# Performance work log

Measured on AMD Instinct MI355X. Metric: run time of the kernel, lower is better.

Reference implementation:

```python
import jax, jax.numpy as jnp
import numpy as np

N, E, D, H_ATT = 10000, 640000, 128, 64


def setup_inputs() -> dict:
    key = jax.random.key(0)
    ks = jax.random.split(key, 8)
    s = 1.0 / np.sqrt(D)
    return {
        "x": jax.random.normal(ks[0], (N, D), jnp.float32),
        "row": jax.random.randint(ks[1], (E,), 0, N, dtype=jnp.int32),
        "col": jax.random.randint(ks[2], (E,), 0, N, dtype=jnp.int32),
        "W1": jax.random.normal(ks[3], (D, D), jnp.float32) * s,
        "b1": jnp.zeros((D,), jnp.float32),
        "W2": jax.random.normal(ks[4], (D, D), jnp.float32) * s,
        "b2": jnp.zeros((D,), jnp.float32),
        "A1": jax.random.normal(ks[5], (D, H_ATT), jnp.float32) * s,
        "ab1": jnp.zeros((H_ATT,), jnp.float32),
        "A2": jax.random.normal(ks[6], (H_ATT, 1), jnp.float32) * (1.0 / np.sqrt(H_ATT)),
    }


def _cos_sim(a, b):
    # torch.cosine_similarity with eps=1e-8
    num = jnp.sum(a * b, axis=-1)
    den = jnp.maximum(jnp.linalg.norm(a, axis=-1) * jnp.linalg.norm(b, axis=-1), 1e-8)
    return num / den


def _euclid(a, b):
    # nn.PairwiseDistance(p=2)
    return jnp.sqrt(jnp.sum((a - b) ** 2, axis=-1) + 1e-12)


def _gcn(x, ew, row, col, W, b):
    # PyG GCNConv: add self loops (weight 1), symmetric normalization, SpMM.
    n = x.shape[0]
    loop = jnp.arange(n, dtype=row.dtype)
    r = jnp.concatenate([row, loop])  # target
    c = jnp.concatenate([col, loop])  # source
    w = jnp.concatenate([ew, jnp.ones((n,), x.dtype)])
    deg = jax.ops.segment_sum(w, r, num_segments=n)
    dis = jnp.where(deg > 0, jax.lax.rsqrt(jnp.maximum(deg, 1e-12)), 0.0)
    norm = dis[r] * w * dis[c]  # [E+N]
    h = x @ W  # [N, out]
    out = jax.ops.segment_sum(norm[:, None] * h[c], r, num_segments=n)
    return out + b


def reference(x, row, col, W1, b1, W2, b2, A1, ab1, A2):
    # --- cosine branch ---
    w = _cos_sim(x[row], x[col])
    x1 = jax.nn.relu(_gcn(x, w, row, col, W1, b1))
    w = _cos_sim(x1[row], x1[col])
    x1 = _gcn(x1, w, row, col, W2, b2)
    # --- euclidean branch ---
    w = _euclid(x[row], x[col])
    x2 = jax.nn.relu(_gcn(x, w, row, col, W1, b1))
    w = _euclid(x2[row], x2[col])
    x2 = _gcn(x2, w, row, col, W2, b2)
    # --- semantic attention fusion ---
    emb = jnp.stack([x1, x2], axis=1)  # [N, 2, D]
    score = jnp.tanh(emb @ A1 + ab1) @ A2  # [N, 2, 1]
    beta = jax.nn.softmax(score, axis=1)
    return jnp.sum(beta * emb, axis=1)  # [N, D]
```

## Files before the change

### kernel.cpp

```cpp
#include <hip/hip_runtime.h>
#include <cstdint>
#include <cstddef>

#define DF 128
#define HATT 64
#define SL 64
#define RPB 1280

static inline int divup(int a, int b) { return (a + b - 1) / b; }

typedef int vint4 __attribute__((ext_vector_type(4)));

__device__ __forceinline__ void warm_table(const float* t, int nf4, int b, int nb) {
    int slice = (nf4 + nb - 1) / nb;
    int start = b * slice;
    int end = min(start + slice, nf4);
    float acc = 0.f;
    for (int i = start + (int)threadIdx.x; i < end; i += 256) {
        float4 v = ((const float4*)t)[i];
        acc += v.x + v.y + v.z + v.w;
    }
    asm volatile("" :: "v"(acc));
}

__device__ __forceinline__ void hist2_body(int bid, const int* __restrict__ row,
                                           int* __restrict__ cnt2,
                                           int E, int n, int ranges, int rpb, int es) {
    int rb = bid % ranges;
    int s  = bid / ranges;
    int lo = rb * rpb, hi = min(lo + rpb, n);
    int rows = hi - lo;
    __shared__ int lc[RPB];
    for (int j = threadIdx.x; j < rows; j += 256) lc[j] = 0;
    __syncthreads();
    int i0 = s * es, i1 = min(i0 + es, E);
    const vint4* rv = (const vint4*)row;
    for (int j = i0 / 4 + threadIdx.x; j < i1 / 4; j += 256) {
        vint4 r4 = __builtin_nontemporal_load(rv + j);
        if (r4.x >= lo && r4.x < hi) atomicAdd(&lc[r4.x - lo], 1);
        if (r4.y >= lo && r4.y < hi) atomicAdd(&lc[r4.y - lo], 1);
        if (r4.z >= lo && r4.z < hi) atomicAdd(&lc[r4.z - lo], 1);
        if (r4.w >= lo && r4.w < hi) atomicAdd(&lc[r4.w - lo], 1);
    }
    __syncthreads();
    for (int j = threadIdx.x; j < rows; j += 256) cnt2[(size_t)s * n + lo + j] = lc[j];
}

__device__ __forceinline__ void split_x_body(int bid, const float* __restrict__ x,
                                             float* __restrict__ xA,
                                             float* __restrict__ xB,
                                             float* __restrict__ sqn, int n) {
    int wid = bid * 4 + (threadIdx.x >> 6);
    int lane = threadIdx.x & 63;
    if (wid >= n) return;
    float v0 = x[(size_t)wid * DF + lane];
    float v1 = x[(size_t)wid * DF + 64 + lane];
    xA[(size_t)wid * 64 + lane] = v0;
    xB[(size_t)wid * 64 + lane] = v1;
    float s = v0 * v0 + v1 * v1;
    for (int off = 32; off; off >>= 1) s += __shfl_xor(s, off);
    if (lane == 0) sqn[wid] = s;
}

__global__ __launch_bounds__(256) void prep_split_kernel(const int* __restrict__ row,
                                                         int* __restrict__ cnt2,
                                                         const float* __restrict__ x,
                                                         float* __restrict__ xA,
                                                         float* __restrict__ xB,
                                                         float* __restrict__ sqn,
                                                         int E, int n, int ranges, int rpb,
                                                         int es, int prepBlocks) {
    if ((int)blockIdx.x < prepBlocks)
        hist2_body(blockIdx.x, row, cnt2, E, n, ranges, rpb, es);
    else
        split_x_body(blockIdx.x - prepBlocks, x, xA, xB, sqn, n);
}

__global__ __launch_bounds__(256) void scanRT_kernel(int* __restrict__ cnt2,
                                                     int* __restrict__ tot, int n) {
    __shared__ int tile[SL][65];
    int r0 = blockIdx.x * 64;
    int w = threadIdx.x >> 6;
    int lane = threadIdx.x & 63;
    int rows = min(64, n - r0);
    for (int s = w; s < SL; s += 4) {
        int v = (lane < rows) ? cnt2[(size_t)s * n + r0 + lane] : 0;
        tile[s][lane] = v;
    }
    __syncthreads();
    int t = threadIdx.x;
    if (t < rows) {
        int run = 0;
#pragma unroll
        for (int s = 0; s < SL; ++s) {
            int v = tile[s][t];
            tile[s][t] = run;
            run += v;
        }
        tot[r0 + t] = run;
    }
    __syncthreads();
    for (int s = w; s < SL; s += 4) {
        if (lane < rows) cnt2[(size_t)s * n + r0 + lane] = tile[s][lane];
    }
}

__global__ __launch_bounds__(1024) void scanT_kernel(const int* __restrict__ tot,
                                                     int* __restrict__ row_ptr, int n) {
    __shared__ int sums[1024];
    int t = threadIdx.x;
    int chunk = (n + 1023) >> 10;
    int start = t * chunk, end = min(start + chunk, n);
    int s = 0;
    for (int r = start; r < end; ++r) s += tot[r];
    sums[t] = s;
    __syncthreads();
    for (int off = 1; off < 1024; off <<= 1) {
        int v = (t >= off) ? sums[t - off] : 0;
        __syncthreads();
        sums[t] += v;
        __syncthreads();
    }
    int run = sums[t] - s;
    for (int r = start; r < end; ++r) {
        row_ptr[r] = run;
        run += tot[r];
    }
    if (t == 1023) row_ptr[n] = sums[1023];
}

__global__ __launch_bounds__(256) void scatter2_kernel(const int* __restrict__ row,
                                                       const int* __restrict__ col,
                                                       const int* __restrict__ cnt2,
                                                       const int* __restrict__ row_ptr,
                                                       unsigned short* __restrict__ col_s,
                                                       int E, int n, int ranges, int rpb, int es) {
    int rb = blockIdx.x % ranges;
    int s  = blockIdx.x / ranges;
    int lo = rb * rpb, hi = min(lo + rpb, n);
    int rows = hi - lo;
    __shared__ int cur[RPB];
    for (int j = threadIdx.x; j < rows; j += 256)
        cur[j] = cnt2[(size_t)s * n + lo + j] + row_ptr[lo + j];
    __syncthreads();
    int i0 = s * es, i1 = min(i0 + es, E);
    const vint4* rv = (const vint4*)row;
    const vint4* cv = (const vint4*)col;
    for (int j = i0 / 4 + threadIdx.x; j < i1 / 4; j += 256) {
        vint4 r4 = __builtin_nontemporal_load(rv + j);
        bool b0 = (r4.x >= lo && r4.x < hi);
        bool b1 = (r4.y >= lo && r4.y < hi);
        bool b2 = (r4.z >= lo && r4.z < hi);
        bool b3 = (r4.w >= lo && r4.w < hi);
        if (b0 | b1 | b2 | b3) {
            vint4 c4 = __builtin_nontemporal_load(cv + j);
            if (b0) { int p = atomicAdd(&cur[r4.x - lo], 1); col_s[p] = (unsigned short)c4.x; }
            if (b1) { int p = atomicAdd(&cur[r4.y - lo], 1); col_s[p] = (unsigned short)c4.y; }
            if (b2) { int p = atomicAdd(&cur[r4.z - lo], 1); col_s[p] = (unsigned short)c4.z; }
            if (b3) { int p = atomicAdd(&cur[r4.w - lo], 1); col_s[p] = (unsigned short)c4.w; }
        }
    }
}

__device__ __forceinline__ void edgewA_body(int bid, const float* __restrict__ tA,
                                            const unsigned short* __restrict__ col_s,
                                            const int* __restrict__ row_ptr,
                                            float* __restrict__ dpart, int n, int nbTable) {
    warm_table(tA, n * 16, bid, nbTable);
    int wid = bid * 4 + (threadIdx.x >> 6);
    int lane = threadIdx.x & 63;
    if (wid >= n) return;
    int sub = lane & 15, g = lane >> 4;
    int s = row_ptr[wid], e = row_ptr[wid + 1];
    float4 a = ((const float4*)(tA + (size_t)wid * 64))[sub];
    for (int base = s; base < e; base += 64) {
        int m = e - base; if (m > 64) m = 64;
        int cc = 0;
        if (lane < m) cc = (int)col_s[base + lane];
        float dkeep = 0.f;
#define EWA_BODY(CHK)                                                        \
        _Pragma("unroll")                                                    \
        for (int it = 0; it < 16; ++it) {                                    \
            int idx = g * 16 + it;                                           \
            int c = __shfl(cc, idx);                                         \
            if (CHK) {                                                       \
                float4 b = ((const float4*)(tA + (size_t)c * 64))[sub];      \
                float d = a.x * b.x + a.y * b.y + a.z * b.z + a.w * b.w;     \
                d += __shfl_xor(d, 8); d += __shfl_xor(d, 4);                \
                d += __shfl_xor(d, 2); d += __shfl_xor(d, 1);                \
                dkeep = (sub == it) ? d : dkeep;                             \
            }                                                                \
        }
        if (m == 64) { EWA_BODY(true) } else { EWA_BODY(idx < m) }
#undef EWA_BODY
        if (lane < m) dpart[base + lane] = dkeep;
    }
}

__device__ __forceinline__ void mm_body(int bid, const float* __restrict__ inA,
                                        const float* __restrict__ inB, int strideIn,
                                        const float* __restrict__ W,
                                        float* __restrict__ hA, float* __restrict__ hB, int n) {
    int wid = bid * 4 + (threadIdx.x >> 6);
    int lane = threadIdx.x & 63;
    int i0 = wid * 4;
    if (i0 >= n) return;
    float v0[4], v1[4];
#pragma unroll
    for (int r = 0; r < 4; ++r) {
        int i = i0 + r;
        if (i < n) { v0[r] = inA[(size_t)i * strideIn + lane]; v1[r] = inB[(size_t)i * strideIn + lane]; }
        else { v0[r] = 0.f; v1[r] = 0.f; }
    }
    float acc0[4] = {0.f, 0.f, 0.f, 0.f};
    float acc1[4] = {0.f, 0.f, 0.f, 0.f};
#pragma unroll 4
    for (int k = 0; k < 64; ++k) {
        float w0 = W[k * DF + lane];
        float w1 = W[k * DF + 64 + lane];
#pragma unroll
        for (int r = 0; r < 4; ++r) {
            float a = __shfl(v0[r], k);
            acc0[r] = fmaf(a, w0, acc0[r]);
            acc1[r] = fmaf(a, w1, acc1[r]);
        }
    }
#pragma unroll 4
    for (int k = 0; k < 64; ++k) {
        float w0 = W[(k + 64) * DF + lane];
        float w1 = W[(k + 64) * DF + 64 + lane];
#pragma unroll
        for (int r = 0; r < 4; ++r) {
            float a = __shfl(v1[r], k);
            acc0[r] = fmaf(a, w0, acc0[r]);
            acc1[r] = fmaf(a, w1, acc1[r]);
        }
    }
#pragma unroll
    for (int r = 0; r < 4; ++r) {
        int i = i0 + r;
        if (i < n) { hA[(size_t)i * 64 + lane] = acc0[r]; hB[(size_t)i * 64 + lane] = acc1[r]; }
    }
}

__global__ __launch_bounds__(256) void ew1mm_kernel(const float* __restrict__ xA,
                                                    const unsigned short* __restrict__ col_s,
                                                    const int* __restrict__ row_ptr,
                                                    float* __restrict__ dp0,
                                                    const float* __restrict__ x,
                                                    const float* __restrict__ W1,
                                                    float* __restrict__ hA,
                                                    float* __restrict__ hB,
                                                    int n, int nodeBlocks) {
    if ((int)blockIdx.x < nodeBlocks)
        edgewA_body(blockIdx.x, xA, col_s, row_ptr, dp0, n, nodeBlocks);
    else
        mm_body(blockIdx.x - nodeBlocks, x, x + 64, DF, W1, hA, hB, n);
}

__global__ __launch_bounds__(256) void edgewB1_kernel(const float* __restrict__ tB,
                                                      const float* __restrict__ sqn,
                                                      const unsigned short* __restrict__ col_s,
                                                      const int* __restrict__ row_ptr,
                                                      const float* __restrict__ dpart,
                                                      float* __restrict__ wA,
                                                      float* __restrict__ wB,
                                                      float* __restrict__ disA,
                                                      float* __restrict__ disB, int n, int nbTable) {
    warm_table(tB, n * 16, blockIdx.x, nbTable);
    int wid = blockIdx.x * 4 + (threadIdx.x >> 6);
    int lane = threadIdx.x & 63;
    if (wid >= n) return;
    int sub = lane & 15, g = lane >> 4;
    int s = row_ptr[wid], e = row_ptr[wid + 1];
    float4 a = ((const float4*)(tB + (size_t)wid * 64))[sub];
    float na = sqn[wid];
    float accA = 0.f, accB = 0.f;
    for (int base = s; base < e; base += 64) {
        int m = e - base; if (m > 64) m = 64;
        int cc = 0; float dp = 0.f;
        if (lane < m) {
            cc = (int)col_s[base + lane];
            dp = dpart[base + lane];
        }
        float dkeep = 0.f;
#define EWB1_BODY(CHK)                                                       \
        _Pragma("unroll")                                                    \
        for (int it = 0; it < 16; ++it) {                                    \
            int idx = g * 16 + it;                                           \
            int c = __shfl(cc, idx);                                         \
            if (CHK) {                                                       \
                float4 b = ((const float4*)(tB + (size_t)c * 64))[sub];      \
                float d = a.x * b.x + a.y * b.y + a.z * b.z + a.w * b.w;     \
                d += __shfl_xor(d, 8); d += __shfl_xor(d, 4);                \
                d += __shfl_xor(d, 2); d += __shfl_xor(d, 1);                \
                dkeep = (sub == it) ? d : dkeep;                             \
            }                                                                \
        }
        if (m == 64) { EWB1_BODY(true) } else { EWB1_BODY(idx < m) }
#undef EWB1_BODY
        if (lane < m) {
            float d = dkeep + dp;
            float nb = sqn[cc];
            float cw = d / fmaxf(sqrtf(na * nb), 1e-8f);
            float ew = sqrtf(fmaxf(na + nb - 2.f * d, 0.f) + 1e-12f);
            wA[base + lane] = cw;
            wB[base + lane] = ew;
            accA += cw;
            accB += ew;
        }
    }
#pragma unroll
    for (int off = 32; off; off >>= 1) {
        accA += __shfl_xor(accA, off);
        accB += __shfl_xor(accB, off);
    }
    if (lane == 0) {
        float dA = 1.f + accA;
        disA[wid] = (dA > 0.f) ? rsqrtf(fmaxf(dA, 1e-12f)) : 0.f;
        float dB = 1.f + accB;
        disB[wid] = (dB > 0.f) ? rsqrtf(fmaxf(dB, 1e-12f)) : 0.f;
    }
}

__global__ __launch_bounds__(256) void spmm_l1_kernel(const float* __restrict__ hA,
                                                      const float* __restrict__ hB,
                                                      const float* __restrict__ wsA,
                                                      const float* __restrict__ wsB,
                                                      const unsigned short* __restrict__ col_s,
                                                      const float* __restrict__ disA,
                                                      const float* __restrict__ disB,
                                                      const int* __restrict__ row_ptr,
                                                      const float* __restrict__ bias,
                                                      float* __restrict__ x1A, float* __restrict__ x1B,
                                                      float* __restrict__ x2A, float* __restrict__ x2B,
                                                      float* __restrict__ sq1pA, float* __restrict__ sq1pB,
                                                      float* __restrict__ sq2pA, float* __restrict__ sq2pB,
                                                      int n, int nbTable) {
    int half = blockIdx.x & 1;
    const float* hH = half ? hB : hA;
    warm_table(hH, n * 16, blockIdx.x >> 1, nbTable);
    int wid = (blockIdx.x >> 1) * 4 + (threadIdx.x >> 6);
    int lane = threadIdx.x & 63;
    if (wid >= n) return;
    float* x1H = half ? x1B : x1A;
    float* x2H = half ? x2B : x2A;
    float* sq1 = half ? sq1pB : sq1pA;
    float* sq2 = half ? sq2pB : sq2pA;
    const float* biasH = bias + half * 64;
    int sub = lane & 15, g = lane >> 4;
    int s = row_ptr[wid], e = row_ptr[wid + 1];
    float diA = disA[wid], diB = disB[wid];
    float4 aA = make_float4(0.f, 0.f, 0.f, 0.f);
    float4 aB = make_float4(0.f, 0.f, 0.f, 0.f);
    for (int base = s; base < e; base += 64) {
        int m = e - base; if (m > 64) m = 64;
        int cc = 0; float wa = 0.f, wb = 0.f;
        if (lane < m) {
            cc = (int)col_s[base + lane];
            wa = wsA[base + lane] * disA[cc];
            wb = wsB[base + lane] * disB[cc];
        }
#define SPL1_BODY(CHK)                                                       \
        _Pragma("unroll")                                                    \
        for (int it = 0; it < 16; ++it) {                                    \
            int idx = it * 4 + g;                                            \
            int c = __shfl(cc, idx);                                         \
            float ceA = __shfl(wa, idx);                                     \
            float ceB = __shfl(wb, idx);                                     \
            if (CHK) {                                                       \
                float4 gv = ((const float4*)(hH + (size_t)c * 64))[sub];     \
                aA.x = fmaf(ceA, gv.x, aA.x); aA.y = fmaf(ceA, gv.y, aA.y);  \
                aA.z = fmaf(ceA, gv.z, aA.z); aA.w = fmaf(ceA, gv.w, aA.w);  \
                aB.x = fmaf(ceB, gv.x, aB.x); aB.y = fmaf(ceB, gv.y, aB.y);  \
                aB.z = fmaf(ceB, gv.z, aB.z); aB.w = fmaf(ceB, gv.w, aB.w);  \
            }                                                                \
        }
        if (m == 64) { SPL1_BODY(true) } else { SPL1_BODY(idx < m) }
#undef SPL1_BODY
    }
#pragma unroll
    for (int off = 16; off <= 32; off <<= 1) {
        aA.x += __shfl_xor(aA.x, off); aA.y += __shfl_xor(aA.y, off);
        aA.z += __shfl_xor(aA.z, off); aA.w += __shfl_xor(aA.w, off);
        aB.x += __shfl_xor(aB.x, off); aB.y += __shfl_xor(aB.y, off);
        aB.z += __shfl_xor(aB.z, off); aB.w += __shfl_xor(aB.w, off);
    }
    float4 hv = ((const float4*)(hH + (size_t)wid * 64))[sub];
    float4 bb = ((const float4*)biasH)[sub];
    float4 oA, oB;
    oA.x = fmaxf(diA * (aA.x + diA * hv.x) + bb.x, 0.f);
    oA.y = fmaxf(diA * (aA.y + diA * hv.y) + bb.y, 0.f);
    oA.z = fmaxf(diA * (aA.z + diA * hv.z) + bb.z, 0.f);
    oA.w = fmaxf(diA * (aA.w + diA * hv.w) + bb.w, 0.f);
    oB.x = fmaxf(diB * (aB.x + diB * hv.x) + bb.x, 0.f);
    oB.y = fmaxf(diB * (aB.y + diB * hv.y) + bb.y, 0.f);
    oB.z = fmaxf(diB * (aB.z + diB * hv.z) + bb.z, 0.f);
    oB.w = fmaxf(diB * (aB.w + diB * hv.w) + bb.w, 0.f);
    if (g == 0) {
        ((float4*)(x1H + (size_t)wid * 64))[sub] = oA;
        ((float4*)(x2H + (size_t)wid * 64))[sub] = oB;
    }
    float sA = oA.x * oA.x + oA.y * oA.y + oA.z * oA.z + oA.w * oA.w;
    float sB = oB.x * oB.x + oB.y * oB.y + oB.z * oB.z + oB.w * oB.w;
#pragma unroll
    for (int off = 8; off; off >>= 1) {
        sA += __shfl_xor(sA, off);
        sB += __shfl_xor(sB, off);
    }
    if (lane == 0) { sq1[wid] = sA; sq2[wid] = sB; }
}

__device__ __forceinline__ void mm2_body(int bid, const float* __restrict__ x1A_,
                                         const float* __restrict__ x1B_,
                                         const float* __restrict__ x2A_,
                                         const float* __restrict__ x2B_,
                                         const float* __restrict__ W,
                                         float* __restrict__ h1A, float* __restrict__ h1B,
                                         float* __restrict__ h2A, float* __restrict__ h2B, int n) {
    int br = bid & 1;
    const float* inA = br ? x2A_ : x1A_;
    const float* inB = br ? x2B_ : x1B_;
    float* hA = br ? h2A : h1A;
    float* hB = br ? h2B : h1B;
    mm_body(bid >> 1, inA, inB, 64, W, hA, hB, n);
}

__global__ __launch_bounds__(256) void ew2mm_kernel(const float* __restrict__ x1A,
                                                    const float* __restrict__ x1B,
                                                    const float* __restrict__ x2A,
                                                    const float* __restrict__ x2B,
                                                    const unsigned short* __restrict__ col_s,
                                                    const int* __restrict__ row_ptr,
                                                    float* __restrict__ dp0,
                                                    float* __restrict__ dp1,
                                                    const float* __restrict__ W2,
                                                    float* __restrict__ h1A, float* __restrict__ h1B,
                                                    float* __restrict__ h2A, float* __restrict__ h2B,
                                                    int n, int pairBlocks, int nodeBlocks) {
    if ((int)blockIdx.x < pairBlocks) {
        int br = blockIdx.x & 1;
        const float* tA = br ? x2A : x1A;
        float* dpart = br ? dp1 : dp0;
        edgewA_body(blockIdx.x >> 1, tA, col_s, row_ptr, dpart, n, nodeBlocks);
    } else {
        mm2_body(blockIdx.x - pairBlocks, x1A, x1B, x2A, x2B, W2, h1A, h1B, h2A, h2B, n);
    }
}

__global__ __launch_bounds__(256) void edgewB2_kernel(const float* __restrict__ t0B,
                                                      const float* __restrict__ t1B,
                                                      const float* __restrict__ sq1pA,
                                                      const float* __restrict__ sq1pB,
                                                      const float* __restrict__ sq2pA,
                                                      const float* __restrict__ sq2pB,
                                                      const unsigned short* __restrict__ col_s,
                                                      const int* __restrict__ row_ptr,
                                                      const float* __restrict__ dp0,
                                                      const float* __restrict__ dp1,
                                                      float* __restrict__ wsA,
                                                      float* __restrict__ wsB,
                                                      float* __restrict__ disA,
                                                      float* __restrict__ disB, int n, int nbTable) {
    int br = blockIdx.x & 1;
    const float* tB = br ? t1B : t0B;
    warm_table(tB, n * 16, blockIdx.x >> 1, nbTable);
    int wid = (blockIdx.x >> 1) * 4 + (threadIdx.x >> 6);
    int lane = threadIdx.x & 63;
    if (wid >= n) return;
    const float* sqA = br ? sq2pA : sq1pA;
    const float* sqB = br ? sq2pB : sq1pB;
    const float* dpart = br ? dp1 : dp0;
    float* wOut = br ? wsB : wsA;
    float* disOut = br ? disB : disA;
    int sub = lane & 15, g = lane >> 4;
    int s = row_ptr[wid], e = row_ptr[wid + 1];
    float4 a = ((const float4*)(tB + (size_t)wid * 64))[sub];
    float na = sqA[wid] + sqB[wid];
    float acc = 0.f;
    for (int base = s; base < e; base += 64) {
        int m = e - base; if (m > 64) m = 64;
        int cc = 0; float dp = 0.f;
        if (lane < m) {
            cc = (int)col_s[base + lane];
            dp = dpart[base + lane];
        }
        float dkeep = 0.f;
#define EWB2_BODY(CHK)                                                       \
        _Pragma("unroll")                                                    \
        for (int it = 0; it < 16; ++it) {                                    \
            int idx = g * 16 + it;                                           \
            int c = __shfl(cc, idx);                                         \
            if (CHK) {                                                       \
                float4 b = ((const float4*)(tB + (size_t)c * 64))[sub];      \
                float d = a.x * b.x + a.y * b.y + a.z * b.z + a.w * b.w;     \
                d += __shfl_xor(d, 8); d += __shfl_xor(d, 4);                \
                d += __shfl_xor(d, 2); d += __shfl_xor(d, 1);                \
                dkeep = (sub == it) ? d : dkeep;                             \
            }                                                                \
        }
        if (m == 64) { EWB2_BODY(true) } else { EWB2_BODY(idx < m) }
#undef EWB2_BODY
        if (lane < m) {
            float d = dkeep + dp;
            float nb = sqA[cc] + sqB[cc];
            float w;
            if (br == 0) w = d / fmaxf(sqrtf(na * nb), 1e-8f);
            else w = sqrtf(fmaxf(na + nb - 2.f * d, 0.f) + 1e-12f);
            wOut[base + lane] = w;
            acc += w;
        }
    }
#pragma unroll
    for (int off = 32; off; off >>= 1) acc += __shfl_xor(acc, off);
    if (lane == 0) {
        float dg = 1.f + acc;
        disOut[wid] = (dg > 0.f) ? rsqrtf(fmaxf(dg, 1e-12f)) : 0.f;
    }
}

__global__ __launch_bounds__(256) void spmm2q_kernel(const float* __restrict__ h1A,
                                                     const float* __restrict__ h1B,
                                                     const float* __restrict__ h2A,
                                                     const float* __restrict__ h2B,
                                                     const float* __restrict__ wsA,
                                                     const float* __restrict__ wsB,
                                                     const unsigned short* __restrict__ col_s,
                                                     const float* __restrict__ disA,
                                                     const float* __restrict__ disB,
                                                     const int* __restrict__ row_ptr,
                                                     const float* __restrict__ bias,
                                                     float* __restrict__ x1A, float* __restrict__ x1B,
                                                     float* __restrict__ x2A, float* __restrict__ x2B,
                                                     int n, int nbTable) {
    int sel = blockIdx.x & 3;
    int br = sel & 1;
    int half = sel >> 1;
    const float* hH = br ? (half ? h2B : h2A) : (half ? h1B : h1A);
    warm_table(hH, n * 16, blockIdx.x >> 2, nbTable);
    const float* ws = br ? wsB : wsA;
    const float* dis = br ? disB : disA;
    float* outH = br ? (half ? x2B : x2A) : (half ? x1B : x1A);
    const float* biasH = bias + half * 64;
    int wid = (blockIdx.x >> 2) * 4 + (threadIdx.x >> 6);
    int lane = threadIdx.x & 63;
    if (wid >= n) return;
    int sub = lane & 15, g = lane >> 4;
    int s = row_ptr[wid], e = row_ptr[wid + 1];
    float di = dis[wid];
    float4 a = make_float4(0.f, 0.f, 0.f, 0.f);
    for (int base = s; base < e; base += 64) {
        int m = e - base; if (m > 64) m = 64;
        int cc = 0; float wv = 0.f;
        if (lane < m) {
            cc = (int)col_s[base + lane];
            wv = ws[base + lane] * dis[cc];
        }
#define SP2_BODY(CHK)                                                        \
        _Pragma("unroll")                                                    \
        for (int it = 0; it < 16; ++it) {                                    \
            int idx = it * 4 + g;                                            \
            int c = __shfl(cc, idx);                                         \
            float ce = __shfl(wv, idx);                                      \
            if (CHK) {                                                       \
                float4 gv = ((const float4*)(hH + (size_t)c * 64))[sub];     \
                a.x = fmaf(ce, gv.x, a.x); a.y = fmaf(ce, gv.y, a.y);        \
                a.z = fmaf(ce, gv.z, a.z); a.w = fmaf(ce, gv.w, a.w);        \
            }                                                                \
        }
        if (m == 64) { SP2_BODY(true) } else { SP2_BODY(idx < m) }
#undef SP2_BODY
    }
#pragma unroll
    for (int off = 16; off <= 32; off <<= 1) {
        a.x += __shfl_xor(a.x, off); a.y += __shfl_xor(a.y, off);
        a.z += __shfl_xor(a.z, off); a.w += __shfl_xor(a.w, off);
    }
    if (g == 0) {
        float4 hv = ((const float4*)(hH + (size_t)wid * 64))[sub];
        float4 bb = ((const float4*)biasH)[sub];
        float4 o;
        o.x = di * (a.x + di * hv.x) + bb.x;
        o.y = di * (a.y + di * hv.y) + bb.y;
        o.z = di * (a.z + di * hv.z) + bb.z;
        o.w = di * (a.w + di * hv.w) + bb.w;
        ((float4*)(outH + (size_t)wid * 64))[sub] = o;
    }
}

__global__ __launch_bounds__(256) void attn_kernel(const float* __restrict__ x1A,
                                                   const float* __restrict__ x1B,
                                                   const float* __restrict__ x2A,
                                                   const float* __restrict__ x2B,
                                                   const float* __restrict__ A1,
                                                   const float* __restrict__ ab1,
                                                   const float* __restrict__ A2,
                                                   float* __restrict__ out, int n) {
    __shared__ float sA1[DF * HATT];
    __shared__ float sA2[HATT];
    __shared__ float sab[HATT];
    int tid = threadIdx.x;
    for (int i = tid; i < DF * HATT; i += 256) sA1[i] = A1[i];
    if (tid < HATT) { sA2[tid] = A2[tid]; sab[tid] = ab1[tid]; }
    __syncthreads();
    int lane = tid & 63;
    int wib = tid >> 6;
    int wid = blockIdx.x * 4 + wib;
    int nw = gridDim.x * 4;
    for (int i = wid; i < n; i += nw) {
        float u0 = x1A[(size_t)i * 64 + lane], u1 = x1B[(size_t)i * 64 + lane];
        float v0 = x2A[(size_t)i * 64 + lane], v1 = x2B[(size_t)i * 64 + lane];
        float acc1 = 0.f, acc2 = 0.f;
#pragma unroll 4
        for (int d = 0; d < 64; ++d) {
            float w = sA1[d * HATT + lane];
            acc1 = fmaf(__shfl(u0, d), w, acc1);
            acc2 = fmaf(__shfl(v0, d), w, acc2);
        }
#pragma unroll 4
        for (int d = 0; d < 64; ++d) {
            float w = sA1[(d + 64) * HATT + lane];
            acc1 = fmaf(__shfl(u1, d), w, acc1);
            acc2 = fmaf(__shfl(v1, d), w, acc2);
        }
        float t1 = tanhf(acc1 + sab[lane]) * sA2[lane];
        float t2 = tanhf(acc2 + sab[lane]) * sA2[lane];
        for (int off = 32; off; off >>= 1) {
            t1 += __shfl_xor(t1, off);
            t2 += __shfl_xor(t2, off);
        }
        float mx = fmaxf(t1, t2);
        float e1 = expf(t1 - mx), e2 = expf(t2 - mx);
        float inv = 1.f / (e1 + e2);
        float be1 = e1 * inv, be2 = e2 * inv;
        out[(size_t)i * DF + lane] = be1 * u0 + be2 * v0;
        out[(size_t)i * DF + 64 + lane] = be1 * u1 + be2 * v1;
    }
}


extern "C" void kernel_launch(void* const* d_in, const int* in_sizes, int n_in,
                              void* d_out, int out_size, void* d_ws, size_t ws_size,
                              hipStream_t stream) {
    const float* x  = (const float*)d_in[0];
    const int* row  = (const int*)d_in[1];
    const int* col  = (const int*)d_in[2];
    const float* W1 = (const float*)d_in[3];
    const float* b1 = (const float*)d_in[4];
    const float* W2 = (const float*)d_in[5];
    const float* b2 = (const float*)d_in[6];
    const float* A1 = (const float*)d_in[7];
    const float* ab1= (const float*)d_in[8];
    const float* A2 = (const float*)d_in[9];
    const int N = in_sizes[0] / DF;
    const int E = in_sizes[1];
    float* out = (float*)d_out;

    char* p = (char*)d_ws;
    auto alloc_b = [&](size_t bytes) -> char* {
        char* r = p;
        p += (bytes + 255) & ~(size_t)255;
        return r;
    };
    float* xA    = (float*)alloc_b((size_t)N * 64 * 4);
    float* xB    = (float*)alloc_b((size_t)N * 64 * 4);
    float* hA    = (float*)alloc_b((size_t)N * 64 * 4);
    float* hB    = (float*)alloc_b((size_t)N * 64 * 4);
    float* h2A   = (float*)alloc_b((size_t)N * 64 * 4);
    float* h2B   = (float*)alloc_b((size_t)N * 64 * 4);
    float* x1A   = (float*)alloc_b((size_t)N * 64 * 4);
    float* x1B   = (float*)alloc_b((size_t)N * 64 * 4);
    float* x2A   = (float*)alloc_b((size_t)N * 64 * 4);
    float* x2B   = (float*)alloc_b((size_t)N * 64 * 4);
    float* wsA   = (float*)alloc_b((size_t)E * 4);
    float* wsB   = (float*)alloc_b((size_t)E * 4);
    float* dp0   = (float*)alloc_b((size_t)E * 4);
    float* dp1   = (float*)alloc_b((size_t)E * 4);
    float* disA  = (float*)alloc_b((size_t)N * 4);
    float* disB  = (float*)alloc_b((size_t)N * 4);
    float* sqnx  = (float*)alloc_b((size_t)N * 4);
    float* sq1pA = (float*)alloc_b((size_t)N * 4);
    float* sq1pB = (float*)alloc_b((size_t)N * 4);
    float* sq2pA = (float*)alloc_b((size_t)N * 4);
    float* sq2pB = (float*)alloc_b((size_t)N * 4);
    int* cnt2    = (int*)alloc_b((size_t)SL * N * 4);
    int* tot     = (int*)alloc_b((size_t)N * 4);
    int* rowptr  = (int*)alloc_b((size_t)(N + 1) * 4);
    unsigned short* col_s = (unsigned short*)alloc_b((size_t)E * 2);
    (void)ws_size; (void)n_in; (void)out_size;

    const int nodeBlocks  = divup(N * 64, 256);
    const int pairBlocks  = 2 * nodeBlocks;
    const int quadBlocks  = 4 * nodeBlocks;
    const int mmBlocks    = divup(divup(N, 4), 4);
    const int mm2Blocks   = 2 * mmBlocks;
    const int ranges = divup(N, RPB);
    const int rpb    = divup(N, ranges);
    int es = divup(E, SL); es = (es + 3) & ~3;
    const int prepBlocks = ranges * SL;

    prep_split_kernel<<<prepBlocks + nodeBlocks, 256, 0, stream>>>(row, cnt2, x, xA, xB, sqnx,
                                                                   E, N, ranges, rpb, es, prepBlocks);
    scanRT_kernel<<<divup(N, 64), 256, 0, stream>>>(cnt2, tot, N);
    scanT_kernel<<<1, 1024, 0, stream>>>(tot, rowptr, N);
    scatter2_kernel<<<prepBlocks, 256, 0, stream>>>(row, col, cnt2, rowptr, col_s, E, N, ranges, rpb, es);

    ew1mm_kernel<<<nodeBlocks + mmBlocks, 256, 0, stream>>>(xA, col_s, rowptr, dp0,
                                                            x, W1, hA, hB, N, nodeBlocks);

    edgewB1_kernel<<<nodeBlocks, 256, 0, stream>>>(xB, sqnx, col_s, rowptr, dp0,
                                                   wsA, wsB, disA, disB, N, nodeBlocks);

    spmm_l1_kernel<<<pairBlocks, 256, 0, stream>>>(hA, hB, wsA, wsB, col_s, disA, disB,
                                                   rowptr, b1, x1A, x1B, x2A, x2B,
                                                   sq1pA, sq1pB, sq2pA, sq2pB, N, nodeBlocks);

    ew2mm_kernel<<<pairBlocks + mm2Blocks, 256, 0, stream>>>(x1A, x1B, x2A, x2B, col_s, rowptr,
                                                             dp0, dp1, W2, hA, hB, h2A, h2B,
                                                             N, pairBlocks, nodeBlocks);

    edgewB2_kernel<<<pairBlocks, 256, 0, stream>>>(x1B, x2B, sq1pA, sq1pB, sq2pA, sq2pB,
                                                   col_s, rowptr, dp0, dp1,
                                                   wsA, wsB, disA, disB, N, nodeBlocks);

    spmm2q_kernel<<<quadBlocks, 256, 0, stream>>>(hA, hB, h2A, h2B, wsA, wsB, col_s,
                                                  disA, disB, rowptr, b2,
                                                  x1A, x1B, x2A, x2B, N, nodeBlocks);

    attn_kernel<<<divup(N, 4), 256, 0, stream>>>(x1A, x1B, x2A, x2B, A1, ab1, A2, out, N);
}
```

Before: 358.7 us.

## Fuse split edge-dot passes into single full-width pass; merge scatter with matmul

The edge dot products were computed in two passes, one per 64-column half of the features (tables A and B), with partial sums written to dp0/dp1 buffers. Each edge-weight kernel now computes the full 128-wide dot in one pass, with half-warps reading A or B and reducing across 32 lanes. The dp buffers, the L2-warming loops and two kernel launches go away. The W1 matmul now runs alongside the CSR scatter instead of the first edge pass, which cuts launch count and partial-sum traffic. The cost is a larger gathered working set per pass, since both halves are read together, and fewer edges handled per shuffle round.

```diff
diff --git a/kernel.cpp b/kernel.cpp
--- a/kernel.cpp
+++ b/kernel.cpp
@@ -129,14 +129,14 @@
     if (t == 1023) row_ptr[n] = sums[1023];
 }
 
-__global__ __launch_bounds__(256) void scatter2_kernel(const int* __restrict__ row,
-                                                       const int* __restrict__ col,
-                                                       const int* __restrict__ cnt2,
-                                                       const int* __restrict__ row_ptr,
-                                                       unsigned short* __restrict__ col_s,
-                                                       int E, int n, int ranges, int rpb, int es) {
-    int rb = blockIdx.x % ranges;
-    int s  = blockIdx.x / ranges;
+__device__ __forceinline__ void scatter2_body(int bid, const int* __restrict__ row,
+                                              const int* __restrict__ col,
+                                              const int* __restrict__ cnt2,
+                                              const int* __restrict__ row_ptr,
+                                              unsigned short* __restrict__ col_s,
+                                              int E, int n, int ranges, int rpb, int es) {
+    int rb = bid % ranges;
+    int s  = bid / ranges;
     int lo = rb * rpb, hi = min(lo + rpb, n);
     int rows = hi - lo;
     __shared__ int cur[RPB];
@@ -162,41 +162,6 @@
     }
 }
 
-__device__ __forceinline__ void edgewA_body(int bid, const float* __restrict__ tA,
-                                            const unsigned short* __restrict__ col_s,
-                                            const int* __restrict__ row_ptr,
-                                            float* __restrict__ dpart, int n, int nbTable) {
-    warm_table(tA, n * 16, bid, nbTable);
-    int wid = bid * 4 + (threadIdx.x >> 6);
-    int lane = threadIdx.x & 63;
-    if (wid >= n) return;
-    int sub = lane & 15, g = lane >> 4;
-    int s = row_ptr[wid], e = row_ptr[wid + 1];
-    float4 a = ((const float4*)(tA + (size_t)wid * 64))[sub];
-    for (int base = s; base < e; base += 64) {
-        int m = e - base; if (m > 64) m = 64;
-        int cc = 0;
-        if (lane < m) cc = (int)col_s[base + lane];
-        float dkeep = 0.f;
-#define EWA_BODY(CHK)                                                        \
-        _Pragma("unroll")                                                    \
-        for (int it = 0; it < 16; ++it) {                                    \
-            int idx = g * 16 + it;                                           \
-            int c = __shfl(cc, idx);                                         \
-            if (CHK) {                                                       \
-                float4 b = ((const float4*)(tA + (size_t)c * 64))[sub];      \
-                float d = a.x * b.x + a.y * b.y + a.z * b.z + a.w * b.w;     \
-                d += __shfl_xor(d, 8); d += __shfl_xor(d, 4);                \
-                d += __shfl_xor(d, 2); d += __shfl_xor(d, 1);                \
-                dkeep = (sub == it) ? d : dkeep;                             \
-            }                                                                \
-        }
-        if (m == 64) { EWA_BODY(true) } else { EWA_BODY(idx < m) }
-#undef EWA_BODY
-        if (lane < m) dpart[base + lane] = dkeep;
-    }
-}
-
 __device__ __forceinline__ void mm_body(int bid, const float* __restrict__ inA,
                                         const float* __restrict__ inB, int strideIn,
                                         const float* __restrict__ W,
@@ -243,64 +208,65 @@
     }
 }
 
-__global__ __launch_bounds__(256) void ew1mm_kernel(const float* __restrict__ xA,
-                                                    const unsigned short* __restrict__ col_s,
-                                                    const int* __restrict__ row_ptr,
-                                                    float* __restrict__ dp0,
-                                                    const float* __restrict__ x,
-                                                    const float* __restrict__ W1,
-                                                    float* __restrict__ hA,
-                                                    float* __restrict__ hB,
-                                                    int n, int nodeBlocks) {
-    if ((int)blockIdx.x < nodeBlocks)
-        edgewA_body(blockIdx.x, xA, col_s, row_ptr, dp0, n, nodeBlocks);
+__global__ __launch_bounds__(256) void scatmm_kernel(const int* __restrict__ row,
+                                                     const int* __restrict__ col,
+                                                     const int* __restrict__ cnt2,
+                                                     const int* __restrict__ row_ptr,
+                                                     unsigned short* __restrict__ col_s,
+                                                     const float* __restrict__ x,
+                                                     const float* __restrict__ W1,
+                                                     float* __restrict__ hA,
+                                                     float* __restrict__ hB,
+                                                     int E, int n, int ranges, int rpb,
+                                                     int es, int prepBlocks) {
+    if ((int)blockIdx.x < prepBlocks)
+        scatter2_body(blockIdx.x, row, col, cnt2, row_ptr, col_s, E, n, ranges, rpb, es);
     else
-        mm_body(blockIdx.x - nodeBlocks, x, x + 64, DF, W1, hA, hB, n);
-}
-
-__global__ __launch_bounds__(256) void edgewB1_kernel(const float* __restrict__ tB,
+        mm_body(blockIdx.x - prepBlocks, x, x + 64, DF, W1, hA, hB, n);
+}
+
+
+__global__ __launch_bounds__(256) void edgew1f_kernel(const float* __restrict__ xA,
+                                                      const float* __restrict__ xB,
                                                       const float* __restrict__ sqn,
                                                       const unsigned short* __restrict__ col_s,
                                                       const int* __restrict__ row_ptr,
-                                                      const float* __restrict__ dpart,
                                                       float* __restrict__ wA,
                                                       float* __restrict__ wB,
                                                       float* __restrict__ disA,
-                                                      float* __restrict__ disB, int n, int nbTable) {
-    warm_table(tB, n * 16, blockIdx.x, nbTable);
+                                                      float* __restrict__ disB, int n) {
     int wid = blockIdx.x * 4 + (threadIdx.x >> 6);
     int lane = threadIdx.x & 63;
     if (wid >= n) return;
-    int sub = lane & 15, g = lane >> 4;
+    int sub = lane & 15;
+    const float* tH = ((lane >> 4) & 1) ? xB : xA;
     int s = row_ptr[wid], e = row_ptr[wid + 1];
-    float4 a = ((const float4*)(tB + (size_t)wid * 64))[sub];
+    float4 a = ((const float4*)(tH + (size_t)wid * 64))[sub];
     float na = sqn[wid];
     float accA = 0.f, accB = 0.f;
     for (int base = s; base < e; base += 64) {
         int m = e - base; if (m > 64) m = 64;
-        int cc = 0; float dp = 0.f;
-        if (lane < m) {
-            cc = (int)col_s[base + lane];
-            dp = dpart[base + lane];
-        }
+        int cc = 0;
+        if (lane < m) cc = (int)col_s[base + lane];
         float dkeep = 0.f;
-#define EWB1_BODY(CHK)                                                       \
+#define EW1F_BODY(CHK)                                                       \
         _Pragma("unroll")                                                    \
-        for (int it = 0; it < 16; ++it) {                                    \
-            int idx = g * 16 + it;                                           \
+        for (int it = 0; it < 32; ++it) {                                    \
+            int idx = (lane & 32) + it;                                      \
             int c = __shfl(cc, idx);                                         \
             if (CHK) {                                                       \
-                float4 b = ((const float4*)(tB + (size_t)c * 64))[sub];      \
+                float4 b = ((const float4*)(tH + (size_t)c * 64))[sub];      \
                 float d = a.x * b.x + a.y * b.y + a.z * b.z + a.w * b.w;     \
-                d += __shfl_xor(d, 8); d += __shfl_xor(d, 4);                \
-                d += __shfl_xor(d, 2); d += __shfl_xor(d, 1);                \
-                dkeep = (sub == it) ? d : dkeep;                             \
+                d += __shfl_xor(d, 16); d += __shfl_xor(d, 8);               \
+                d += __shfl_xor(d, 4);  d += __shfl_xor(d, 2);               \
+                d += __shfl_xor(d, 1);                                       \
+                dkeep = ((lane & 31) == it) ? d : dkeep;                     \
             }                                                                \
         }
-        if (m == 64) { EWB1_BODY(true) } else { EWB1_BODY(idx < m) }
-#undef EWB1_BODY
+        if (m == 64) { EW1F_BODY(true) } else { EW1F_BODY(idx < m) }
+#undef EW1F_BODY
         if (lane < m) {
-            float d = dkeep + dp;
+            float d = dkeep;
             float nb = sqn[cc];
             float cw = d / fmaxf(sqrtf(na * nb), 1e-8f);
             float ew = sqrtf(fmaxf(na + nb - 2.f * d, 0.f) + 1e-12f);
@@ -320,6 +286,107 @@
         disA[wid] = (dA > 0.f) ? rsqrtf(fmaxf(dA, 1e-12f)) : 0.f;
         float dB = 1.f + accB;
         disB[wid] = (dB > 0.f) ? rsqrtf(fmaxf(dB, 1e-12f)) : 0.f;
+    }
+}
+
+__device__ __forceinline__ void edgew2f_body(int bid, int br,
+                                             const float* __restrict__ tAt,
+                                             const float* __restrict__ tBt,
+                                             const float* __restrict__ sqA,
+                                             const float* __restrict__ sqB,
+                                             const unsigned short* __restrict__ col_s,
+                                             const int* __restrict__ row_ptr,
+                                             float* __restrict__ wOut,
+                                             float* __restrict__ disOut, int n) {
+    int wid = bid * 4 + (threadIdx.x >> 6);
+    int lane = threadIdx.x & 63;
+    if (wid >= n) return;
+    int sub = lane & 15;
+    const float* tH = ((lane >> 4) & 1) ? tBt : tAt;
+    int s = row_ptr[wid], e = row_ptr[wid + 1];
+    float4 a = ((const float4*)(tH + (size_t)wid * 64))[sub];
+    float na = sqA[wid] + sqB[wid];
+    float acc = 0.f;
+    for (int base = s; base < e; base += 64) {
+        int m = e - base; if (m > 64) m = 64;
+        int cc = 0;
+        if (lane < m) cc = (int)col_s[base + lane];
+        float dkeep = 0.f;
+#define EW2F_BODY(CHK)                                                       \
+        _Pragma("unroll")                                                    \
+        for (int it = 0; it < 32; ++it) {                                    \
+            int idx = (lane & 32) + it;                                      \
+            int c = __shfl(cc, idx);                                         \
+            if (CHK) {                                                       \
+                float4 b = ((const float4*)(tH + (size_t)c * 64))[sub];      \
+                float d = a.x * b.x + a.y * b.y + a.z * b.z + a.w * b.w;     \
+                d += __shfl_xor(d, 16); d += __shfl_xor(d, 8);               \
+                d += __shfl_xor(d, 4);  d += __shfl_xor(d, 2);               \
+                d += __shfl_xor(d, 1);                                       \
+                dkeep = ((lane & 31) == it) ? d : dkeep;                     \
+            }                                                                \
+        }
+        if (m == 64) { EW2F_BODY(true) } else { EW2F_BODY(idx < m) }
+#undef EW2F_BODY
+        if (lane < m) {
+            float d = dkeep;
+            float nb = sqA[cc] + sqB[cc];
+            float w;
+            if (br == 0) w = d / fmaxf(sqrtf(na * nb), 1e-8f);
+            else w = sqrtf(fmaxf(na + nb - 2.f * d, 0.f) + 1e-12f);
+            wOut[base + lane] = w;
+            acc += w;
+        }
+    }
+#pragma unroll
+    for (int off = 32; off; off >>= 1) acc += __shfl_xor(acc, off);
+    if (lane == 0) {
+        float dg = 1.f + acc;
+        disOut[wid] = (dg > 0.f) ? rsqrtf(fmaxf(dg, 1e-12f)) : 0.f;
+    }
+}
+
+__device__ __forceinline__ void mm2_body(int bid, const float* __restrict__ x1A_,
+                                         const float* __restrict__ x1B_,
+                                         const float* __restrict__ x2A_,
+                                         const float* __restrict__ x2B_,
+                                         const float* __restrict__ W,
+                                         float* __restrict__ h1A, float* __restrict__ h1B,
+                                         float* __restrict__ h2A, float* __restrict__ h2B, int n) {
+    int br = bid & 1;
+    const float* inA = br ? x2A_ : x1A_;
+    const float* inB = br ? x2B_ : x1B_;
+    float* hA = br ? h2A : h1A;
+    float* hB = br ? h2B : h1B;
+    mm_body(bid >> 1, inA, inB, 64, W, hA, hB, n);
+}
+
+__global__ __launch_bounds__(256) void ew2mm2_kernel(const float* __restrict__ x1A,
+                                                     const float* __restrict__ x1B,
+                                                     const float* __restrict__ x2A,
+                                                     const float* __restrict__ x2B,
+                                                     const float* __restrict__ sq1pA,
+                                                     const float* __restrict__ sq1pB,
+                                                     const float* __restrict__ sq2pA,
+                                                     const float* __restrict__ sq2pB,
+                                                     const unsigned short* __restrict__ col_s,
+                                                     const int* __restrict__ row_ptr,
+                                                     float* __restrict__ wsA,
+                                                     float* __restrict__ wsB,
+                                                     float* __restrict__ disA,
+                                                     float* __restrict__ disB,
+                                                     const float* __restrict__ W2,
+                                                     float* __restrict__ h1A, float* __restrict__ h1B,
+                                                     float* __restrict__ h2A, float* __restrict__ h2B,
+                                                     int n, int pairBlocks) {
+    if ((int)blockIdx.x < pairBlocks) {
+        int br = blockIdx.x & 1;
+        if (br == 0)
+            edgew2f_body(blockIdx.x >> 1, 0, x1A, x1B, sq1pA, sq1pB, col_s, row_ptr, wsA, disA, n);
+        else
+            edgew2f_body(blockIdx.x >> 1, 1, x2A, x2B, sq2pA, sq2pB, col_s, row_ptr, wsB, disB, n);
+    } else {
+        mm2_body(blockIdx.x - pairBlocks, x1A, x1B, x2A, x2B, W2, h1A, h1B, h2A, h2B, n);
     }
 }
 
@@ -411,114 +478,6 @@
     if (lane == 0) { sq1[wid] = sA; sq2[wid] = sB; }
 }
 
-__device__ __forceinline__ void mm2_body(int bid, const float* __restrict__ x1A_,
-                                         const float* __restrict__ x1B_,
-                                         const float* __restrict__ x2A_,
-                                         const float* __restrict__ x2B_,
-                                         const float* __restrict__ W,
-                                         float* __restrict__ h1A, float* __restrict__ h1B,
-                                         float* __restrict__ h2A, float* __restrict__ h2B, int n) {
-    int br = bid & 1;
-    const float* inA = br ? x2A_ : x1A_;
-    const float* inB = br ? x2B_ : x1B_;
-    float* hA = br ? h2A : h1A;
-    float* hB = br ? h2B : h1B;
-    mm_body(bid >> 1, inA, inB, 64, W, hA, hB, n);
-}
-
-__global__ __launch_bounds__(256) void ew2mm_kernel(const float* __restrict__ x1A,
-                                                    const float* __restrict__ x1B,
-                                                    const float* __restrict__ x2A,
-                                                    const float* __restrict__ x2B,
-                                                    const unsigned short* __restrict__ col_s,
-                                                    const int* __restrict__ row_ptr,
-                                                    float* __restrict__ dp0,
-                                                    float* __restrict__ dp1,
-                                                    const float* __restrict__ W2,
-                                                    float* __restrict__ h1A, float* __restrict__ h1B,
-                                                    float* __restrict__ h2A, float* __restrict__ h2B,
-                                                    int n, int pairBlocks, int nodeBlocks) {
-    if ((int)blockIdx.x < pairBlocks) {
-        int br = blockIdx.x & 1;
-        const float* tA = br ? x2A : x1A;
-        float* dpart = br ? dp1 : dp0;
-        edgewA_body(blockIdx.x >> 1, tA, col_s, row_ptr, dpart, n, nodeBlocks);
-    } else {
-        mm2_body(blockIdx.x - pairBlocks, x1A, x1B, x2A, x2B, W2, h1A, h1B, h2A, h2B, n);
-    }
-}
-
-__global__ __launch_bounds__(256) void edgewB2_kernel(const float* __restrict__ t0B,
-                                                      const float* __restrict__ t1B,
-                                                      const float* __restrict__ sq1pA,
-                                                      const float* __restrict__ sq1pB,
-                                                      const float* __restrict__ sq2pA,
-                                                      const float* __restrict__ sq2pB,
-                                                      const unsigned short* __restrict__ col_s,
-                                                      const int* __restrict__ row_ptr,
-                                                      const float* __restrict__ dp0,
-                                                      const float* __restrict__ dp1,
-                                                      float* __restrict__ wsA,
-                                                      float* __restrict__ wsB,
-                                                      float* __restrict__ disA,
-                                                      float* __restrict__ disB, int n, int nbTable) {
-    int br = blockIdx.x & 1;
-    const float* tB = br ? t1B : t0B;
-    warm_table(tB, n * 16, blockIdx.x >> 1, nbTable);
-    int wid = (blockIdx.x >> 1) * 4 + (threadIdx.x >> 6);
-    int lane = threadIdx.x & 63;
-    if (wid >= n) return;
-    const float* sqA = br ? sq2pA : sq1pA;
-    const float* sqB = br ? sq2pB : sq1pB;
-    const float* dpart = br ? dp1 : dp0;
-    float* wOut = br ? wsB : wsA;
-    float* disOut = br ? disB : disA;
-    int sub = lane & 15, g = lane >> 4;
-    int s = row_ptr[wid], e = row_ptr[wid + 1];
-    float4 a = ((const float4*)(tB + (size_t)wid * 64))[sub];
-    float na = sqA[wid] + sqB[wid];
-    float acc = 0.f;
-    for (int base = s; base < e; base += 64) {
-        int m = e - base; if (m > 64) m = 64;
-        int cc = 0; float dp = 0.f;
-        if (lane < m) {
-            cc = (int)col_s[base + lane];
-            dp = dpart[base + lane];
-        }
-        float dkeep = 0.f;
-#define EWB2_BODY(CHK)                                                       \
-        _Pragma("unroll")                                                    \
-        for (int it = 0; it < 16; ++it) {                                    \
-            int idx = g * 16 + it;                                           \
-            int c = __shfl(cc, idx);                                         \
-            if (CHK) {                                                       \
-                float4 b = ((const float4*)(tB + (size_t)c * 64))[sub];      \
-                float d = a.x * b.x + a.y * b.y + a.z * b.z + a.w * b.w;     \
-                d += __shfl_xor(d, 8); d += __shfl_xor(d, 4);                \
-                d += __shfl_xor(d, 2); d += __shfl_xor(d, 1);                \
-                dkeep = (sub == it) ? d : dkeep;                             \
-            }                                                                \
-        }
-        if (m == 64) { EWB2_BODY(true) } else { EWB2_BODY(idx < m) }
-#undef EWB2_BODY
-        if (lane < m) {
-            float d = dkeep + dp;
-            float nb = sqA[cc] + sqB[cc];
-            float w;
-            if (br == 0) w = d / fmaxf(sqrtf(na * nb), 1e-8f);
-            else w = sqrtf(fmaxf(na + nb - 2.f * d, 0.f) + 1e-12f);
-            wOut[base + lane] = w;
-            acc += w;
-        }
-    }
-#pragma unroll
-    for (int off = 32; off; off >>= 1) acc += __shfl_xor(acc, off);
-    if (lane == 0) {
-        float dg = 1.f + acc;
-        disOut[wid] = (dg > 0.f) ? rsqrtf(fmaxf(dg, 1e-12f)) : 0.f;
-    }
-}
-
 __global__ __launch_bounds__(256) void spmm2q_kernel(const float* __restrict__ h1A,
                                                      const float* __restrict__ h1B,
                                                      const float* __restrict__ h2A,
@@ -674,8 +633,6 @@
     float* x2B   = (float*)alloc_b((size_t)N * 64 * 4);
     float* wsA   = (float*)alloc_b((size_t)E * 4);
     float* wsB   = (float*)alloc_b((size_t)E * 4);
-    float* dp0   = (float*)alloc_b((size_t)E * 4);
-    float* dp1   = (float*)alloc_b((size_t)E * 4);
     float* disA  = (float*)alloc_b((size_t)N * 4);
     float* disB  = (float*)alloc_b((size_t)N * 4);
     float* sqnx  = (float*)alloc_b((size_t)N * 4);
@@ -703,25 +660,24 @@
                                                                    E, N, ranges, rpb, es, prepBlocks);
     scanRT_kernel<<<divup(N, 64), 256, 0, stream>>>(cnt2, tot, N);
     scanT_kernel<<<1, 1024, 0, stream>>>(tot, rowptr, N);
-    scatter2_kernel<<<prepBlocks, 256, 0, stream>>>(row, col, cnt2, rowptr, col_s, E, N, ranges, rpb, es);
-
-    ew1mm_kernel<<<nodeBlocks + mmBlocks, 256, 0, stream>>>(xA, col_s, rowptr, dp0,
-                                                            x, W1, hA, hB, N, nodeBlocks);
-
-    edgewB1_kernel<<<nodeBlocks, 256, 0, stream>>>(xB, sqnx, col_s, rowptr, dp0,
-                                                   wsA, wsB, disA, disB, N, nodeBlocks);
+
+    scatmm_kernel<<<prepBlocks + mmBlocks, 256, 0, stream>>>(row, col, cnt2, rowptr, col_s,
+                                                             x, W1, hA, hB,
+                                                             E, N, ranges, rpb, es, prepBlocks);
+
+    edgew1f_kernel<<<nodeBlocks, 256, 0, stream>>>(xA, xB, sqnx, col_s, rowptr,
+                                                   wsA, wsB, disA, disB, N);
 
     spmm_l1_kernel<<<pairBlocks, 256, 0, stream>>>(hA, hB, wsA, wsB, col_s, disA, disB,
                                                    rowptr, b1, x1A, x1B, x2A, x2B,
                                                    sq1pA, sq1pB, sq2pA, sq2pB, N, nodeBlocks);
 
-    ew2mm_kernel<<<pairBlocks + mm2Blocks, 256, 0, stream>>>(x1A, x1B, x2A, x2B, col_s, rowptr,
-                                                             dp0, dp1, W2, hA, hB, h2A, h2B,
-                                                             N, pairBlocks, nodeBlocks);
-
-    edgewB2_kernel<<<pairBlocks, 256, 0, stream>>>(x1B, x2B, sq1pA, sq1pB, sq2pA, sq2pB,
-                                                   col_s, rowptr, dp0, dp1,
-                                                   wsA, wsB, disA, disB, N, nodeBlocks);
+    ew2mm2_kernel<<<pairBlocks + mm2Blocks, 256, 0, stream>>>(x1A, x1B, x2A, x2B,
+                                                              sq1pA, sq1pB, sq2pA, sq2pB,
+                                                              col_s, rowptr,
+                                                              wsA, wsB, disA, disB,
+                                                              W2, hA, hB, h2A, h2B,
+                                                              N, pairBlocks);
 
     spmm2q_kernel<<<quadBlocks, 256, 0, stream>>>(hA, hB, h2A, h2B, wsA, wsB, col_s,
                                                   disA, disB, rowptr, b2,
```

Measured after the change: 411.7 us. +14.8%, slower.
